# Optimization experiments

Hardware: AMD Instinct MI355X
Metric: run time of the kernel (lower is better)

## Reference

```python
import jax, jax.numpy as jnp
import numpy as np


def setup_inputs() -> dict:
    key = jax.random.key(0)
    k1, k2 = jax.random.split(key)
    x = jax.random.normal(k1, (8, 32, 252, 252), dtype=jnp.float32)
    weight = jax.random.normal(k2, (32, 32, 5, 5), dtype=jnp.float32)
    return {"x": x, "weight": weight}


def reference(x, weight):
    # FFT-based conv2d, mathematically identical to the torch module but with
    # the batch-invariant weight FFT hoisted out of the batch dimension.
    k = weight.shape[-1]
    p = k // 2
    # reflect padding (matches F.pad mode='reflect')
    xp = jnp.pad(x, ((0, 0), (0, 0), (p, p), (p, p)), mode="reflect")
    H, W = xp.shape[-2], xp.shape[-1]
    # embed kernel in top-left of a full-size zero canvas, then circular roll
    # by (-k)//2 (Python floor division, as in the original torch code)
    wp = jnp.zeros((weight.shape[0], weight.shape[1], H, W), dtype=x.dtype)
    wp = wp.at[:, :, :k, :k].set(weight)
    shift = (-k) // 2  # e.g. k=5 -> -3, matching torch.roll(shifts=(-k//2,...))
    wp = jnp.roll(wp, shift=(shift, shift), axis=(-2, -1))
    x_fft = jnp.fft.fft2(xp)          # [B, I, H, W] complex
    w_fft = jnp.fft.fft2(wp)          # [O, I, H, W] complex (no batch copy)
    out_fft = jnp.einsum("bihw,oihw->bohw", x_fft, w_fft)
    out = jnp.fft.ifft2(out_fft).real
    return out[:, :, p:-p, p:-p]
```

## Files before the change

### kernel.cpp

```cpp
#include <hip/hip_runtime.h>

typedef __attribute__((ext_vector_type(8))) short bf16x8;
typedef __attribute__((ext_vector_type(4))) float f32x4;

#define HW_   252
#define PLANE 63504
#define NCH   32
#define PADW  262
#define PROW  (PADW * NCH)
#define PIMG  ((size_t)PADW * PROW)
#define XPAD_ELEMS ((size_t)8 * PIMG)
#define WP_OFF_BYTES (XPAD_ELEMS * 2)
#define WS_NEED (WP_OFF_BYTES + 25600u * 2u)

__device__ __forceinline__ unsigned short f2bf(float f) {
    unsigned u = __builtin_bit_cast(unsigned, f);
    u += 0x7FFFu + ((u >> 16) & 1u);
    return (unsigned short)(u >> 16);
}

__device__ __forceinline__ int refl(int p) {
    int t = (p & 255) - 2;
    t = t < 0 ? -t : t;
    return t > 251 ? 502 - t : t;
}

__global__ __launch_bounds__(256) void pad_pack(
    const float* __restrict__ x, unsigned short* __restrict__ xp,
    const float* __restrict__ w, unsigned short* __restrict__ wp)
{
    const int bid = blockIdx.x;
    const int tid = threadIdx.x;

    if (bid >= 8 * PADW) {
        int e = (bid - 8 * PADW) * 256 + tid;
        int ci = e & 31;
        int o  = (e >> 5) & 31;
        int t  = e >> 10;
        int da = t / 5, db = t - da * 5;
        wp[e] = f2bf(w[((o * 32 + ci) * 5 + (4 - da)) * 5 + (4 - db)]);
        return;
    }

    __shared__ unsigned short s[32][260];

    const int b  = bid / PADW;
    const int r  = bid - b * PADW;
    const int mr = refl(r);
    const float* src0 = x + (size_t)b * NCH * PLANE + (size_t)mr * HW_;

    {
        const int ci   = tid >> 3;
        const int part = tid & 7;
        const float* sp = src0 + (size_t)ci * PLANE;
        #pragma unroll
        for (int c4 = 0; c4 < 8; ++c4) {
            int col = part * 32 + c4 * 4;
            if (col < HW_) {
                float4 v = *reinterpret_cast<const float4*>(sp + col);
                s[ci][col + 0] = f2bf(v.x);
                s[ci][col + 1] = f2bf(v.y);
                s[ci][col + 2] = f2bf(v.z);
                s[ci][col + 3] = f2bf(v.w);
            }
        }
    }
    __syncthreads();

    unsigned short* dst0 = xp + (size_t)b * PIMG + (size_t)r * PROW;
    const int cpart = tid >> 2;
    const int g     = tid & 3;
    #pragma unroll
    for (int cb = 0; cb < PADW; cb += 64) {
        int c = cb + cpart;
        if (c < PADW) {
            int mc = refl(c);
            unsigned short pk[8];
            #pragma unroll
            for (int q = 0; q < 8; ++q) pk[q] = s[g * 8 + q][mc];
            *reinterpret_cast<uint4*>(dst0 + (size_t)c * NCH + g * 8) =
                *reinterpret_cast<const uint4*>(pk);
        }
    }
}

__global__ __launch_bounds__(256, 4) void conv_mfma_v5(
    const unsigned short* __restrict__ xp,
    const unsigned short* __restrict__ wp,
    float* __restrict__ out)
{
    __shared__ unsigned short xl[32 * 20 * 32];

    const int tid  = threadIdx.x;
    const int orig = blockIdx.x;
    const int b    = orig & 7;
    const int idx  = orig >> 3;
    const int rt   = idx >> 4;
    const int ct   = idx & 15;
    const int i0 = rt * 28, j0 = ct * 16;

    const int lane = tid & 63;
    const int wid  = tid >> 6;

    {
        const char* gb = (const char*)(xp +
            ((size_t)b * PIMG + (size_t)(i0 + 1) * PROW + (size_t)(j0 + 1) * NCH));
        #pragma unroll
        for (int it = 0; it < 10; ++it) {
            int unit = it * 256 + tid;
            int pr   = unit / 80;
            int u    = unit - pr * 80;
            const char* src = gb + (size_t)pr * (PROW * 2) + u * 16;
            char* ldst = ((char*)xl) + (it * 4096 + wid * 1024);
            __builtin_amdgcn_global_load_lds(
                (const __attribute__((address_space(1))) void*)src,
                (__attribute__((address_space(3))) void*)ldst,
                16, 0, 0);
        }
    }
    __syncthreads();

    const int lm   = lane & 15;
    const int lg   = lane >> 4;
    const int rowb = wid * 7;

    const char* xlb = reinterpret_cast<const char*>(xl);
    const char* wb  = reinterpret_cast<const char*>(wp);
    const int afix  = (lm << 6) + (lg << 4);
    const int j     = j0 + lm;

    f32x4 acc[7][2];
    #pragma unroll
    for (int r = 0; r < 7; ++r) {
        acc[r][0] = (f32x4){0.f, 0.f, 0.f, 0.f};
        acc[r][1] = (f32x4){0.f, 0.f, 0.f, 0.f};
    }

    #pragma unroll
    for (int db = 0; db < 5; ++db) {
        bf16x8 a[5][2];
        #pragma unroll
        for (int da = 0; da < 5; ++da) {
            const char* ap = wb + ((da * 5 + db) << 11) + afix;
            a[da][0] = *reinterpret_cast<const bf16x8*>(ap);
            a[da][1] = *reinterpret_cast<const bf16x8*>(ap + 1024);
        }

        #pragma unroll
        for (int l = 0; l < 11; ++l) {
            bf16x8 bf = *reinterpret_cast<const bf16x8*>(
                xlb + (rowb + l) * 1280 + ((lm + db) << 6) + (lg << 4));
            #pragma unroll
            for (int da = 0; da < 5; ++da) {
                const int r = l - da;
                if (r >= 0 && r < 7) {
                    acc[r][0] = __builtin_amdgcn_mfma_f32_16x16x32_bf16(
                        a[da][0], bf, acc[r][0], 0, 0, 0);
                    acc[r][1] = __builtin_amdgcn_mfma_f32_16x16x32_bf16(
                        a[da][1], bf, acc[r][1], 0, 0, 0);
                }
            }
        }
    }

    #pragma unroll
    for (int r = 0; r < 7; ++r) {
        const int i = i0 + rowb + r;
        if (j < HW_) {
            #pragma unroll
            for (int mt = 0; mt < 2; ++mt) {
                size_t rowoff = ((size_t)(b * NCH + mt * 16 + lg * 4)) * PLANE
                              + (size_t)i * HW_ + j;
                #pragma unroll
                for (int q = 0; q < 4; ++q)
                    out[rowoff + (size_t)q * PLANE] = acc[r][mt][q];
            }
        }
    }
}

__global__ __launch_bounds__(256) void conv_mfma_fb(
    const float* __restrict__ x,
    const float* __restrict__ w_raw,
    float* __restrict__ out)
{
    __shared__ unsigned short xl[12800];
    __shared__ unsigned short wl[25600];
    __shared__ int rmap[20], cmap[20];

    const int tid = threadIdx.x;
    const int bid = blockIdx.x;
    const int b  = bid >> 8;
    const int rt = (bid >> 4) & 15;
    const int ct = bid & 15;
    const int i0 = rt * 16, j0 = ct * 16;

    if (tid < 40) {
        int k    = tid < 20 ? tid : tid - 20;
        int base = tid < 20 ? i0  : j0;
        int r = (base + 1 + k) & 255;
        int t = r - 2;
        int m = t < 0 ? -t : (t > 251 ? 502 - t : t);
        if (tid < 20) rmap[k] = m; else cmap[k] = m;
    }
    for (int e = tid; e < 25600; e += 256) {
        int o   = e / 800;
        int rem = e - o * 800;
        int ci  = rem / 25;
        int kd  = rem - ci * 25;
        wl[(24 - kd) * 1024 + o * 32 + ci] = f2bf(w_raw[e]);
    }
    __syncthreads();

    for (int task = tid; task < 1600; task += 256) {
        int col = task % 20;
        int g   = (task / 20) & 3;
        int row = task / 80;
        const float* src = x + (size_t)(b * NCH + g * 8) * PLANE
                             + (size_t)rmap[row] * HW_ + cmap[col];
        unsigned short pk[8];
        #pragma unroll
        for (int q = 0; q < 8; ++q) pk[q] = f2bf(src[q * PLANE]);
        int off = ((row * 20 + col) << 6) + ((g ^ (col & 3)) << 4);
        *reinterpret_cast<uint4*>(reinterpret_cast<char*>(xl) + off)
            = *reinterpret_cast<const uint4*>(pk);
    }
    __syncthreads();

    const int lane  = tid & 63;
    const int wid   = tid >> 6;
    const int lm    = lane & 15;
    const int lg    = lane >> 4;
    const int rbase = wid * 4;

    f32x4 acc[4][2];
    #pragma unroll
    for (int rr = 0; rr < 4; ++rr) {
        acc[rr][0] = (f32x4){0.f, 0.f, 0.f, 0.f};
        acc[rr][1] = (f32x4){0.f, 0.f, 0.f, 0.f};
    }

    const char* wbase = (const char*)wl;
    const int afix = (lm << 6) + (lg << 4);
    const char* xlb = reinterpret_cast<const char*>(xl);

    #pragma unroll
    for (int da = 0; da < 5; ++da) {
        #pragma unroll
        for (int db = 0; db < 5; ++db) {
            const int t = da * 5 + db;
            bf16x8 a0 = *reinterpret_cast<const bf16x8*>(wbase + (t << 11) + afix);
            bf16x8 a1 = *reinterpret_cast<const bf16x8*>(wbase + (t << 11) + 1024 + afix);
            const int col  = lm + db;
            const int coff = (col << 6) + ((lg ^ (col & 3)) << 4);
            #pragma unroll
            for (int rr = 0; rr < 4; ++rr) {
                const int row = rbase + rr + da;
                bf16x8 bf = *reinterpret_cast<const bf16x8*>(xlb + row * 1280 + coff);
                acc[rr][0] = __builtin_amdgcn_mfma_f32_16x16x32_bf16(a0, bf, acc[rr][0], 0, 0, 0);
                acc[rr][1] = __builtin_amdgcn_mfma_f32_16x16x32_bf16(a1, bf, acc[rr][1], 0, 0, 0);
            }
        }
    }

    const int j = j0 + lm;
    #pragma unroll
    for (int rr = 0; rr < 4; ++rr) {
        const int i = i0 + rbase + rr;
        if (i < HW_ && j < HW_) {
            size_t rowoff = (size_t)(b * NCH) * PLANE + (size_t)i * HW_ + j;
            #pragma unroll
            for (int mt = 0; mt < 2; ++mt)
                #pragma unroll
                for (int q = 0; q < 4; ++q) {
                    int o = mt * 16 + lg * 4 + q;
                    out[rowoff + (size_t)o * PLANE] = acc[rr][mt][q];
                }
        }
    }
}

extern "C" void kernel_launch(void* const* d_in, const int* in_sizes, int n_in,
                              void* d_out, int out_size, void* d_ws, size_t ws_size,
                              hipStream_t stream) {
    const float* x = (const float*)d_in[0];
    const float* w = (const float*)d_in[1];
    float* out = (float*)d_out;

    if (ws_size >= WS_NEED) {
        unsigned short* xpad = (unsigned short*)d_ws;
        unsigned short* wp   = (unsigned short*)((char*)d_ws + WP_OFF_BYTES);
        hipLaunchKernelGGL(pad_pack, dim3(8 * PADW + 100), dim3(256), 0, stream,
                           x, xpad, w, wp);
        hipLaunchKernelGGL(conv_mfma_v5, dim3(1152), dim3(256), 0, stream,
                           (const unsigned short*)xpad, (const unsigned short*)wp, out);
    } else {
        hipLaunchKernelGGL(conv_mfma_fb, dim3(2048), dim3(256), 0, stream, x, w, out);
    }
}
```

Before: 53.93 us.

## Fuse reflect-pad and bf16 conversion into the conv kernel's tile load

Removes the separate pad_pack pass that wrote a padded, channel-last bf16 copy of the whole input to workspace. The conv kernel now reads fp32 input directly, applies reflect indexing through small shared-memory row and column maps, and converts to bf16 while staging its tile into LDS. Weight packing moves to its own small kernel. This avoids a full write and re-read of the padded intermediate, but the tile loads become strided scalar gathers across channel planes instead of contiguous async global-to-LDS copies. Occupancy hint drops from 4 to 3 blocks.

```diff
diff --git a/kernel.cpp b/kernel.cpp
--- a/kernel.cpp
+++ b/kernel.cpp
@@ -1,4 +1,5 @@
 #include <hip/hip_runtime.h>
+#include <hip/hip_bf16.h>
 
 typedef __attribute__((ext_vector_type(8))) short bf16x8;
 typedef __attribute__((ext_vector_type(4))) float f32x4;
@@ -6,12 +7,7 @@
 #define HW_   252
 #define PLANE 63504
 #define NCH   32
-#define PADW  262
-#define PROW  (PADW * NCH)
-#define PIMG  ((size_t)PADW * PROW)
-#define XPAD_ELEMS ((size_t)8 * PIMG)
-#define WP_OFF_BYTES (XPAD_ELEMS * 2)
-#define WS_NEED (WP_OFF_BYTES + 25600u * 2u)
+#define WS_NEED (25600u * 2u)
 
 __device__ __forceinline__ unsigned short f2bf(float f) {
     unsigned u = __builtin_bit_cast(unsigned, f);
@@ -19,77 +15,23 @@
     return (unsigned short)(u >> 16);
 }
 
-__device__ __forceinline__ int refl(int p) {
-    int t = (p & 255) - 2;
-    t = t < 0 ? -t : t;
-    return t > 251 ? 502 - t : t;
-}
-
-__global__ __launch_bounds__(256) void pad_pack(
-    const float* __restrict__ x, unsigned short* __restrict__ xp,
-    const float* __restrict__ w, unsigned short* __restrict__ wp)
-{
-    const int bid = blockIdx.x;
-    const int tid = threadIdx.x;
-
-    if (bid >= 8 * PADW) {
-        int e = (bid - 8 * PADW) * 256 + tid;
-        int ci = e & 31;
-        int o  = (e >> 5) & 31;
-        int t  = e >> 10;
-        int da = t / 5, db = t - da * 5;
-        wp[e] = f2bf(w[((o * 32 + ci) * 5 + (4 - da)) * 5 + (4 - db)]);
-        return;
-    }
-
-    __shared__ unsigned short s[32][260];
-
-    const int b  = bid / PADW;
-    const int r  = bid - b * PADW;
-    const int mr = refl(r);
-    const float* src0 = x + (size_t)b * NCH * PLANE + (size_t)mr * HW_;
-
-    {
-        const int ci   = tid >> 3;
-        const int part = tid & 7;
-        const float* sp = src0 + (size_t)ci * PLANE;
-        #pragma unroll
-        for (int c4 = 0; c4 < 8; ++c4) {
-            int col = part * 32 + c4 * 4;
-            if (col < HW_) {
-                float4 v = *reinterpret_cast<const float4*>(sp + col);
-                s[ci][col + 0] = f2bf(v.x);
-                s[ci][col + 1] = f2bf(v.y);
-                s[ci][col + 2] = f2bf(v.z);
-                s[ci][col + 3] = f2bf(v.w);
-            }
-        }
-    }
-    __syncthreads();
-
-    unsigned short* dst0 = xp + (size_t)b * PIMG + (size_t)r * PROW;
-    const int cpart = tid >> 2;
-    const int g     = tid & 3;
-    #pragma unroll
-    for (int cb = 0; cb < PADW; cb += 64) {
-        int c = cb + cpart;
-        if (c < PADW) {
-            int mc = refl(c);
-            unsigned short pk[8];
-            #pragma unroll
-            for (int q = 0; q < 8; ++q) pk[q] = s[g * 8 + q][mc];
-            *reinterpret_cast<uint4*>(dst0 + (size_t)c * NCH + g * 8) =
-                *reinterpret_cast<const uint4*>(pk);
-        }
-    }
-}
-
-__global__ __launch_bounds__(256, 4) void conv_mfma_v5(
-    const unsigned short* __restrict__ xp,
+__global__ void pack_w_kernel(const float* __restrict__ w, unsigned short* __restrict__ wp) {
+    int e = blockIdx.x * 256 + threadIdx.x;
+    if (e >= 25600) return;
+    int ci = e & 31;
+    int o  = (e >> 5) & 31;
+    int t  = e >> 10;
+    int da = t / 5, db = t - da * 5;
+    wp[e] = f2bf(w[((o * 32 + ci) * 5 + (4 - da)) * 5 + (4 - db)]);
+}
+
+__global__ __launch_bounds__(256, 3) void conv_fused(
+    const float* __restrict__ x,
     const unsigned short* __restrict__ wp,
     float* __restrict__ out)
 {
     __shared__ unsigned short xl[32 * 20 * 32];
+    __shared__ int rmap[32], cmap[20];
 
     const int tid  = threadIdx.x;
     const int orig = blockIdx.x;
@@ -99,27 +41,40 @@
     const int ct   = idx & 15;
     const int i0 = rt * 28, j0 = ct * 16;
 
+    if (tid < 52) {
+        int k    = tid < 32 ? tid : tid - 32;
+        int base = tid < 32 ? i0  : j0;
+        int r = (base + 1 + k) & 255;
+        int t = r - 2;
+        int m = t < 0 ? -t : (t > 251 ? 502 - t : t);
+        if (tid < 32) rmap[k] = m; else cmap[k] = m;
+    }
+    __syncthreads();
+
+    {
+        const float* xb = x + (size_t)b * NCH * PLANE;
+        #pragma unroll
+        for (int it = 0; it < 10; ++it) {
+            int task = it * 256 + tid;
+            int g    = task & 3;
+            int pc   = task >> 2;
+            int pr   = pc / 20;
+            int col  = pc - pr * 20;
+            const float* src = xb + (size_t)(g * 8) * PLANE
+                                  + (size_t)rmap[pr] * HW_ + cmap[col];
+            unsigned short pk[8];
+            #pragma unroll
+            for (int q = 0; q < 8; ++q)
+                pk[q] = __builtin_bit_cast(unsigned short,
+                            __float2bfloat16(src[q * PLANE]));
+            *reinterpret_cast<uint4*>(reinterpret_cast<char*>(xl) + task * 16)
+                = *reinterpret_cast<const uint4*>(pk);
+        }
+    }
+    __syncthreads();
+
     const int lane = tid & 63;
     const int wid  = tid >> 6;
-
-    {
-        const char* gb = (const char*)(xp +
-            ((size_t)b * PIMG + (size_t)(i0 + 1) * PROW + (size_t)(j0 + 1) * NCH));
-        #pragma unroll
-        for (int it = 0; it < 10; ++it) {
-            int unit = it * 256 + tid;
-            int pr   = unit / 80;
-            int u    = unit - pr * 80;
-            const char* src = gb + (size_t)pr * (PROW * 2) + u * 16;
-            char* ldst = ((char*)xl) + (it * 4096 + wid * 1024);
-            __builtin_amdgcn_global_load_lds(
-                (const __attribute__((address_space(1))) void*)src,
-                (__attribute__((address_space(3))) void*)ldst,
-                16, 0, 0);
-        }
-    }
-    __syncthreads();
-
     const int lm   = lane & 15;
     const int lg   = lane >> 4;
     const int rowb = wid * 7;
@@ -288,12 +243,10 @@
     float* out = (float*)d_out;
 
     if (ws_size >= WS_NEED) {
-        unsigned short* xpad = (unsigned short*)d_ws;
-        unsigned short* wp   = (unsigned short*)((char*)d_ws + WP_OFF_BYTES);
-        hipLaunchKernelGGL(pad_pack, dim3(8 * PADW + 100), dim3(256), 0, stream,
-                           x, xpad, w, wp);
-        hipLaunchKernelGGL(conv_mfma_v5, dim3(1152), dim3(256), 0, stream,
-                           (const unsigned short*)xpad, (const unsigned short*)wp, out);
+        unsigned short* wp = (unsigned short*)d_ws;
+        hipLaunchKernelGGL(pack_w_kernel, dim3(100), dim3(256), 0, stream, w, wp);
+        hipLaunchKernelGGL(conv_fused, dim3(1152), dim3(256), 0, stream,
+                           x, (const unsigned short*)wp, out);
     } else {
         hipLaunchKernelGGL(conv_mfma_fb, dim3(2048), dim3(256), 0, stream, x, w, out);
     }
```

New measurement: 46.65 us. 13.5% less time.

## Read input tiles directly from global, swap MFMA operands for vectorized stores

Applied to the files above, without the earlier changes.

Removes the LDS staging of the padded input tile and the block-wide barrier, so each lane loads its B fragment straight from global memory (relying on L1/L2 for reuse across the 5x5 taps). The MFMA operand order is swapped so each lane holds four consecutive output columns, which lets the epilogue write float4 stores instead of scalar strided stores. Occupancy hint is lowered from 4 to 3 blocks per SM. The cost is more global/cache traffic for overlapping input rows and a coarser boundary check (jq+3<HW) on the output columns.

```diff
diff --git a/kernel.cpp b/kernel.cpp
--- a/kernel.cpp
+++ b/kernel.cpp
@@ -84,13 +84,11 @@
     }
 }
 
-__global__ __launch_bounds__(256, 4) void conv_mfma_v5(
+__global__ __launch_bounds__(256, 3) void conv_v7(
     const unsigned short* __restrict__ xp,
     const unsigned short* __restrict__ wp,
     float* __restrict__ out)
 {
-    __shared__ unsigned short xl[32 * 20 * 32];
-
     const int tid  = threadIdx.x;
     const int orig = blockIdx.x;
     const int b    = orig & 7;
@@ -101,33 +99,15 @@
 
     const int lane = tid & 63;
     const int wid  = tid >> 6;
-
-    {
-        const char* gb = (const char*)(xp +
-            ((size_t)b * PIMG + (size_t)(i0 + 1) * PROW + (size_t)(j0 + 1) * NCH));
-        #pragma unroll
-        for (int it = 0; it < 10; ++it) {
-            int unit = it * 256 + tid;
-            int pr   = unit / 80;
-            int u    = unit - pr * 80;
-            const char* src = gb + (size_t)pr * (PROW * 2) + u * 16;
-            char* ldst = ((char*)xl) + (it * 4096 + wid * 1024);
-            __builtin_amdgcn_global_load_lds(
-                (const __attribute__((address_space(1))) void*)src,
-                (__attribute__((address_space(3))) void*)ldst,
-                16, 0, 0);
-        }
-    }
-    __syncthreads();
-
     const int lm   = lane & 15;
     const int lg   = lane >> 4;
     const int rowb = wid * 7;
 
-    const char* xlb = reinterpret_cast<const char*>(xl);
+    const char* bbase = reinterpret_cast<const char*>(
+        xp + ((size_t)(b * PADW + i0 + 1 + rowb) * PADW + (j0 + 1 + lm)) * NCH
+           + (lg << 3));
     const char* wb  = reinterpret_cast<const char*>(wp);
     const int afix  = (lm << 6) + (lg << 4);
-    const int j     = j0 + lm;
 
     f32x4 acc[7][2];
     #pragma unroll
@@ -149,31 +129,31 @@
         #pragma unroll
         for (int l = 0; l < 11; ++l) {
             bf16x8 bf = *reinterpret_cast<const bf16x8*>(
-                xlb + (rowb + l) * 1280 + ((lm + db) << 6) + (lg << 4));
+                bbase + (size_t)l * (PROW * 2) + db * (NCH * 2));
             #pragma unroll
             for (int da = 0; da < 5; ++da) {
                 const int r = l - da;
                 if (r >= 0 && r < 7) {
                     acc[r][0] = __builtin_amdgcn_mfma_f32_16x16x32_bf16(
-                        a[da][0], bf, acc[r][0], 0, 0, 0);
+                        bf, a[da][0], acc[r][0], 0, 0, 0);
                     acc[r][1] = __builtin_amdgcn_mfma_f32_16x16x32_bf16(
-                        a[da][1], bf, acc[r][1], 0, 0, 0);
+                        bf, a[da][1], acc[r][1], 0, 0, 0);
                 }
             }
         }
     }
 
-    #pragma unroll
-    for (int r = 0; r < 7; ++r) {
-        const int i = i0 + rowb + r;
-        if (j < HW_) {
+    const int jq = j0 + (lg << 2);
+    if (jq + 3 < HW_) {
+        #pragma unroll
+        for (int r = 0; r < 7; ++r) {
+            const int i = i0 + rowb + r;
             #pragma unroll
             for (int mt = 0; mt < 2; ++mt) {
-                size_t rowoff = ((size_t)(b * NCH + mt * 16 + lg * 4)) * PLANE
-                              + (size_t)i * HW_ + j;
-                #pragma unroll
-                for (int q = 0; q < 4; ++q)
-                    out[rowoff + (size_t)q * PLANE] = acc[r][mt][q];
+                float* dst = out + ((size_t)(b * NCH + mt * 16 + lm)) * PLANE
+                           + (size_t)i * HW_ + jq;
+                *reinterpret_cast<float4*>(dst) =
+                    *reinterpret_cast<const float4*>(&acc[r][mt]);
             }
         }
     }
@@ -292,7 +272,7 @@
         unsigned short* wp   = (unsigned short*)((char*)d_ws + WP_OFF_BYTES);
         hipLaunchKernelGGL(pad_pack, dim3(8 * PADW + 100), dim3(256), 0, stream,
                            x, xpad, w, wp);
-        hipLaunchKernelGGL(conv_mfma_v5, dim3(1152), dim3(256), 0, stream,
+        hipLaunchKernelGGL(conv_v7, dim3(1152), dim3(256), 0, stream,
                            (const unsigned short*)xpad, (const unsigned short*)wp, out);
     } else {
         hipLaunchKernelGGL(conv_mfma_fb, dim3(2048), dim3(256), 0, stream, x, w, out);
```

Measured after the change: 70.33 us. +30.4%, slower.
